# Optimization experiments

Measured on AMD Instinct MI355X. Metric: run time of the kernel, lower is better.

The kernel has to match this reference:

```python
import jax, jax.numpy as jnp
import numpy as np

N = 131072          # number of input points
M = 512             # num_prototypes
D = 64              # feature_dim
GAMMA = 1.0


def setup_inputs() -> dict:
    key = jax.random.key(0)
    kx, kp = jax.random.split(key)
    x = jax.random.normal(kx, (N, D), dtype=jnp.float32)
    prototypes = jax.random.normal(kp, (M, D), dtype=jnp.float32)
    return {"x": x, "prototypes": prototypes}


def reference(x, prototypes):
    x_sq = jnp.sum(x * x, axis=-1, keepdims=True)            # [N, 1]
    p_sq = jnp.sum(prototypes * prototypes, axis=-1)         # [M]
    cross = jnp.einsum('nd,md->nm', x, prototypes)           # [N, M]
    dist2 = x_sq + p_sq[None, :] - 2.0 * cross               # [N, M]
    dist2 = jnp.maximum(dist2, 0.0)                          # guard tiny negatives
    return jnp.exp(-GAMMA * dist2)
```

## Files before the change

### kernel.cpp

```cpp
#include <hip/hip_runtime.h>


#define N_PTS 131072
#define M_PROT 512
#define D_DIM 64

typedef __attribute__((ext_vector_type(8))) short short8;
typedef __attribute__((ext_vector_type(4))) float f32x4;

union FragU { uint u[4]; short8 s; };

__device__ inline void load_split(const float* p, short8& hi, short8& lo, float& nrm) {
  const float4 a = *reinterpret_cast<const float4*>(p);
  const float4 b = *reinterpret_cast<const float4*>(p + 4);
  const float f[8] = {a.x, a.y, a.z, a.w, b.x, b.y, b.z, b.w};
  FragU H, L;
#pragma unroll
  for (int i = 0; i < 4; ++i) {
    const uint u0 = __float_as_uint(f[2 * i]);
    const uint u1 = __float_as_uint(f[2 * i + 1]);
    H.u[i] = (u0 >> 16) | (u1 & 0xFFFF0000u);
    const float l0 = f[2 * i]     - __uint_as_float(u0 & 0xFFFF0000u);
    const float l1 = f[2 * i + 1] - __uint_as_float(u1 & 0xFFFF0000u);
    L.u[i] = (__float_as_uint(l0) >> 16) | (__float_as_uint(l1) & 0xFFFF0000u);
    nrm = fmaf(f[2 * i], f[2 * i], nrm);
    nrm = fmaf(f[2 * i + 1], f[2 * i + 1], nrm);
  }
  hi = H.s;
  lo = L.s;
}

__global__ __launch_bounds__(256, 3)
void rbf_mfma(const float* __restrict__ x,
              const float* __restrict__ prot,
              float* __restrict__ out) {
  const int tid = threadIdx.x;
  const int lane = tid & 63;
  const int w = tid >> 6;

  const int bid = blockIdx.x;
  const int wg = (bid & 7) * 512 + (bid >> 3);
  const int ntile = wg >> 2;
  const int mtile = wg & 3;
  const int n0w = ntile * 128 + (w >> 1) * 64;
  const int m0w = mtile * 128 + (w & 1) * 64;

  const int lr = lane & 15;
  const int kg = (lane >> 4) * 8;

  f32x4 acc[4][4];
#pragma unroll
  for (int i = 0; i < 4; ++i)
#pragma unroll
    for (int j = 0; j < 4; ++j) acc[i][j] = (f32x4){0.f, 0.f, 0.f, 0.f};

  float ps_part[4] = {0.f, 0.f, 0.f, 0.f};
  float xs_part[4] = {0.f, 0.f, 0.f, 0.f};

#pragma unroll
  for (int h = 0; h < 2; ++h) {
    short8 PH[4], PL[4], XH[4], XL[4];
#pragma unroll
    for (int fi = 0; fi < 4; ++fi) {
      const float* src = prot + (size_t)(m0w + fi * 16 + lr) * D_DIM + h * 32 + kg;
      load_split(src, PH[fi], PL[fi], ps_part[fi]);
    }
#pragma unroll
    for (int fj = 0; fj < 4; ++fj) {
      const float* src = x + (size_t)(n0w + fj * 16 + lr) * D_DIM + h * 32 + kg;
      load_split(src, XH[fj], XL[fj], xs_part[fj]);
    }
#pragma unroll
    for (int fi = 0; fi < 4; ++fi)
#pragma unroll
      for (int fj = 0; fj < 4; ++fj)
        acc[fi][fj] = __builtin_amdgcn_mfma_f32_16x16x32_bf16(PH[fi], XH[fj], acc[fi][fj], 0, 0, 0);
#pragma unroll
    for (int fi = 0; fi < 4; ++fi)
#pragma unroll
      for (int fj = 0; fj < 4; ++fj)
        acc[fi][fj] = __builtin_amdgcn_mfma_f32_16x16x32_bf16(PH[fi], XL[fj], acc[fi][fj], 0, 0, 0);
#pragma unroll
    for (int fi = 0; fi < 4; ++fi)
#pragma unroll
      for (int fj = 0; fj < 4; ++fj)
        acc[fi][fj] = __builtin_amdgcn_mfma_f32_16x16x32_bf16(PL[fi], XH[fj], acc[fi][fj], 0, 0, 0);
  }

#pragma unroll
  for (int f = 0; f < 4; ++f) {
    ps_part[f] += __shfl_xor(ps_part[f], 16);
    ps_part[f] += __shfl_xor(ps_part[f], 32);
    xs_part[f] += __shfl_xor(xs_part[f], 16);
    xs_part[f] += __shfl_xor(xs_part[f], 32);
  }
  f32x4 psv[4];
#pragma unroll
  for (int fi = 0; fi < 4; ++fi)
#pragma unroll
    for (int r = 0; r < 4; ++r)
      psv[fi][r] = __shfl(ps_part[fi], (lane >> 4) * 4 + r);

#pragma unroll
  for (int fi = 0; fi < 4; ++fi) {
#pragma unroll
    for (int fj = 0; fj < 4; ++fj) {
      const f32x4 c = acc[fi][fj];
      const float xsv = xs_part[fj];
      float4 e;
      e.x = __expf(fminf(fmaf(2.f, c[0], -xsv) - psv[fi][0], 0.f));
      e.y = __expf(fminf(fmaf(2.f, c[1], -xsv) - psv[fi][1], 0.f));
      e.z = __expf(fminf(fmaf(2.f, c[2], -xsv) - psv[fi][2], 0.f));
      e.w = __expf(fminf(fmaf(2.f, c[3], -xsv) - psv[fi][3], 0.f));
      float* addr = out + (size_t)(n0w + fj * 16 + lr) * M_PROT + m0w + fi * 16 + (lane >> 4) * 4;
      *reinterpret_cast<float4*>(addr) = e;
    }
  }
}

extern "C" void kernel_launch(void* const* d_in, const int* in_sizes, int n_in,
                              void* d_out, int out_size, void* d_ws, size_t ws_size,
                              hipStream_t stream) {
  const float* x = (const float*)d_in[0];
  const float* p = (const float*)d_in[1];
  float* out = (float*)d_out;
  (void)in_sizes; (void)n_in; (void)out_size; (void)d_ws; (void)ws_size;
  rbf_mfma<<<(N_PTS / 128) * (M_PROT / 128), 256, 0, stream>>>(x, p, out);
}
```

Baseline: 381.0 us.

## Stage output tile in LDS with swizzle for fully coalesced row stores

```diff
diff --git a/kernel.cpp b/kernel.cpp
--- a/kernel.cpp
+++ b/kernel.cpp
@@ -4,6 +4,7 @@
 #define N_PTS 131072
 #define M_PROT 512
 #define D_DIM 64
+#define BN 32
 
 typedef __attribute__((ext_vector_type(8))) short short8;
 typedef __attribute__((ext_vector_type(4))) float f32x4;
@@ -30,91 +31,92 @@
   lo = L.s;
 }
 
-__global__ __launch_bounds__(256, 3)
+__global__ __launch_bounds__(256, 2)
 void rbf_mfma(const float* __restrict__ x,
               const float* __restrict__ prot,
               float* __restrict__ out) {
+  __shared__ float T[BN * M_PROT];
+
   const int tid = threadIdx.x;
   const int lane = tid & 63;
   const int w = tid >> 6;
-
-  const int bid = blockIdx.x;
-  const int wg = (bid & 7) * 512 + (bid >> 3);
-  const int ntile = wg >> 2;
-  const int mtile = wg & 3;
-  const int n0w = ntile * 128 + (w >> 1) * 64;
-  const int m0w = mtile * 128 + (w & 1) * 64;
-
+  const int n0 = blockIdx.x * BN;
   const int lr = lane & 15;
   const int kg = (lane >> 4) * 8;
+  const int m0w = w * 128;
 
-  f32x4 acc[4][4];
+  f32x4 acc[8][2];
 #pragma unroll
-  for (int i = 0; i < 4; ++i)
+  for (int i = 0; i < 8; ++i)
 #pragma unroll
-    for (int j = 0; j < 4; ++j) acc[i][j] = (f32x4){0.f, 0.f, 0.f, 0.f};
+    for (int j = 0; j < 2; ++j) acc[i][j] = (f32x4){0.f, 0.f, 0.f, 0.f};
 
-  float ps_part[4] = {0.f, 0.f, 0.f, 0.f};
-  float xs_part[4] = {0.f, 0.f, 0.f, 0.f};
+  float ps_part[8] = {0.f, 0.f, 0.f, 0.f, 0.f, 0.f, 0.f, 0.f};
+  float xs_part[2] = {0.f, 0.f};
 
 #pragma unroll
   for (int h = 0; h < 2; ++h) {
-    short8 PH[4], PL[4], XH[4], XL[4];
+    short8 XH[2], XL[2];
 #pragma unroll
-    for (int fi = 0; fi < 4; ++fi) {
-      const float* src = prot + (size_t)(m0w + fi * 16 + lr) * D_DIM + h * 32 + kg;
-      load_split(src, PH[fi], PL[fi], ps_part[fi]);
+    for (int fj = 0; fj < 2; ++fj)
+      load_split(x + (size_t)(n0 + fj * 16 + lr) * D_DIM + h * 32 + kg,
+                 XH[fj], XL[fj], xs_part[fj]);
+#pragma unroll
+    for (int fi = 0; fi < 8; ++fi) {
+      short8 ph, pl;
+      load_split(prot + (size_t)(m0w + fi * 16 + lr) * D_DIM + h * 32 + kg,
+                 ph, pl, ps_part[fi]);
+#pragma unroll
+      for (int fj = 0; fj < 2; ++fj) {
+        acc[fi][fj] = __builtin_amdgcn_mfma_f32_16x16x32_bf16(ph, XH[fj], acc[fi][fj], 0, 0, 0);
+        acc[fi][fj] = __builtin_amdgcn_mfma_f32_16x16x32_bf16(ph, XL[fj], acc[fi][fj], 0, 0, 0);
+        acc[fi][fj] = __builtin_amdgcn_mfma_f32_16x16x32_bf16(pl, XH[fj], acc[fi][fj], 0, 0, 0);
+      }
     }
-#pragma unroll
-    for (int fj = 0; fj < 4; ++fj) {
-      const float* src = x + (size_t)(n0w + fj * 16 + lr) * D_DIM + h * 32 + kg;
-      load_split(src, XH[fj], XL[fj], xs_part[fj]);
-    }
-#pragma unroll
-    for (int fi = 0; fi < 4; ++fi)
-#pragma unroll
-      for (int fj = 0; fj < 4; ++fj)
-        acc[fi][fj] = __builtin_amdgcn_mfma_f32_16x16x32_bf16(PH[fi], XH[fj], acc[fi][fj], 0, 0, 0);
-#pragma unroll
-    for (int fi = 0; fi < 4; ++fi)
-#pragma unroll
-      for (int fj = 0; fj < 4; ++fj)
-        acc[fi][fj] = __builtin_amdgcn_mfma_f32_16x16x32_bf16(PH[fi], XL[fj], acc[fi][fj], 0, 0, 0);
-#pragma unroll
-    for (int fi = 0; fi < 4; ++fi)
-#pragma unroll
-      for (int fj = 0; fj < 4; ++fj)
-        acc[fi][fj] = __builtin_amdgcn_mfma_f32_16x16x32_bf16(PL[fi], XH[fj], acc[fi][fj], 0, 0, 0);
   }
 
 #pragma unroll
-  for (int f = 0; f < 4; ++f) {
-    ps_part[f] += __shfl_xor(ps_part[f], 16);
-    ps_part[f] += __shfl_xor(ps_part[f], 32);
-    xs_part[f] += __shfl_xor(xs_part[f], 16);
-    xs_part[f] += __shfl_xor(xs_part[f], 32);
+  for (int fi = 0; fi < 8; ++fi) {
+    ps_part[fi] += __shfl_xor(ps_part[fi], 16);
+    ps_part[fi] += __shfl_xor(ps_part[fi], 32);
   }
-  f32x4 psv[4];
 #pragma unroll
-  for (int fi = 0; fi < 4; ++fi)
-#pragma unroll
-    for (int r = 0; r < 4; ++r)
-      psv[fi][r] = __shfl(ps_part[fi], (lane >> 4) * 4 + r);
+  for (int fj = 0; fj < 2; ++fj) {
+    xs_part[fj] += __shfl_xor(xs_part[fj], 16);
+    xs_part[fj] += __shfl_xor(xs_part[fj], 32);
+  }
+  const int src = (lane >> 4) * 4;
 
 #pragma unroll
-  for (int fi = 0; fi < 4; ++fi) {
+  for (int fi = 0; fi < 8; ++fi) {
+    f32x4 psv;
 #pragma unroll
-    for (int fj = 0; fj < 4; ++fj) {
+    for (int r = 0; r < 4; ++r) psv[r] = __shfl(ps_part[fi], src + r);
+#pragma unroll
+    for (int fj = 0; fj < 2; ++fj) {
       const f32x4 c = acc[fi][fj];
       const float xsv = xs_part[fj];
       float4 e;
-      e.x = __expf(fminf(fmaf(2.f, c[0], -xsv) - psv[fi][0], 0.f));
-      e.y = __expf(fminf(fmaf(2.f, c[1], -xsv) - psv[fi][1], 0.f));
-      e.z = __expf(fminf(fmaf(2.f, c[2], -xsv) - psv[fi][2], 0.f));
-      e.w = __expf(fminf(fmaf(2.f, c[3], -xsv) - psv[fi][3], 0.f));
-      float* addr = out + (size_t)(n0w + fj * 16 + lr) * M_PROT + m0w + fi * 16 + (lane >> 4) * 4;
-      *reinterpret_cast<float4*>(addr) = e;
+      e.x = __expf(fminf(fmaf(2.f, c[0], -xsv) - psv[0], 0.f));
+      e.y = __expf(fminf(fmaf(2.f, c[1], -xsv) - psv[1], 0.f));
+      e.z = __expf(fminf(fmaf(2.f, c[2], -xsv) - psv[2], 0.f));
+      e.w = __expf(fminf(fmaf(2.f, c[3], -xsv) - psv[3], 0.f));
+      const int n_rel = fj * 16 + lr;
+      const int m = m0w + fi * 16 + src;
+      const int byte = (n_rel * 2048 + m * 4) ^ ((n_rel & 7) << 4);
+      *reinterpret_cast<float4*>(reinterpret_cast<char*>(T) + byte) = e;
     }
+  }
+  __syncthreads();
+
+  const size_t outbase = (size_t)n0 * M_PROT;
+#pragma unroll
+  for (int i = 0; i < 16; ++i) {
+    const int fidx = i * 1024 + tid * 4;
+    const int n_rel = fidx >> 9;
+    const int byte = (fidx * 4) ^ ((n_rel & 7) << 4);
+    const float4 v = *reinterpret_cast<const float4*>(reinterpret_cast<const char*>(T) + byte);
+    *reinterpret_cast<float4*>(out + outbase + fidx) = v;
   }
 }
 
@@ -125,5 +127,5 @@
   const float* p = (const float*)d_in[1];
   float* out = (float*)d_out;
   (void)in_sizes; (void)n_in; (void)out_size; (void)d_ws; (void)ws_size;
-  rbf_mfma<<<(N_PTS / 128) * (M_PROT / 128), 256, 0, stream>>>(x, p, out);
+  rbf_mfma<<<N_PTS / BN, 256, 0, stream>>>(x, p, out);
 }
```

After: 348.0 us. -8.7%, faster.
